# Optimization experiments

Hardware: AMD Instinct MI355X
Metric: run time of the kernel (lower is better)

## Reference

```python
import jax, jax.numpy as jnp
import numpy as np

ALPHA = 0.2  # leaky relu slope
NEG_BIG = -9000000000000000.0


def setup_inputs() -> dict:
    key = jax.random.key(0)
    k1, k2, k3, k4 = jax.random.split(key, 4)
    B, N, Fin, Fout = 8, 2048, 256, 256
    h = jax.random.normal(k1, (B, N, Fin), dtype=jnp.float32)
    adj = jax.random.randint(k2, (B, N, N), 0, 2, dtype=jnp.int32)
    # xavier_uniform with gain=1.414
    gain = 1.414
    limW = gain * np.sqrt(6.0 / (Fin + Fout))
    W = jax.random.uniform(k3, (Fin, Fout), dtype=jnp.float32, minval=-limW, maxval=limW)
    lima = gain * np.sqrt(6.0 / (2 * Fout + 1))
    a = jax.random.uniform(k4, (2 * Fout, 1), dtype=jnp.float32, minval=-lima, maxval=lima)
    return {"h": h, "adj": adj, "W": W, "a": a}


def reference(h, adj, W, a):
    # Wh: [B, N, F]
    Wh = jnp.matmul(h, W)
    Fout = W.shape[1]
    a1 = a[:Fout, 0]   # scores for source node i (repeat_interleave side)
    a2 = a[Fout:, 0]   # scores for target node j (repeat side)
    # e[b,i,j] = leakyrelu(Wh[b,i]@a1 + Wh[b,j]@a2)  -- decomposed, no O(N^2 * 2F) tensor
    s1 = jnp.einsum('bnf,f->bn', Wh, a1)  # [B, N]
    s2 = jnp.einsum('bnf,f->bn', Wh, a2)  # [B, N]
    e = jax.nn.leaky_relu(s1[:, :, None] + s2[:, None, :], negative_slope=ALPHA)
    masked = jnp.where(adj > 0, e, jnp.full_like(e, NEG_BIG))
    attention = jax.nn.softmax(masked, axis=2)  # dropout=0 (eval mode)
    h_prime = jnp.matmul(attention, Wh)  # [B, N, F]
    return jax.nn.elu(h_prime)
```

## Files before the change

kernel.cpp:

```cpp
#include <hip/hip_runtime.h>

typedef __attribute__((ext_vector_type(8))) short bhalf8;
typedef __attribute__((ext_vector_type(4))) float floatx4;

#define ALPHA_LR 0.2f

__device__ __forceinline__ unsigned short f2bf(float f) {
  union { float f; unsigned int u; } v; v.f = f;
  unsigned int r = v.u + 0x7fffu + ((v.u >> 16) & 1u);
  return (unsigned short)(r >> 16);
}
__device__ __forceinline__ float bf2f(unsigned short u) {
  union { unsigned int u; float f; } v; v.u = ((unsigned int)u) << 16;
  return v.f;
}
__device__ __forceinline__ void gld16(const void* g, void* l) {
  __builtin_amdgcn_global_load_lds((const __attribute__((address_space(1))) unsigned int*)g,
                                   (__attribute__((address_space(3))) unsigned int*)l,
                                   16, 0, 0);
}

__global__ void k0w_split(const float* __restrict__ W,
                          unsigned short* __restrict__ WThi,
                          unsigned short* __restrict__ WTlo,
                          unsigned int* __restrict__ s2maxEnc) {
  __shared__ float s[16][17];
  const int tx = threadIdx.x, ty = threadIdx.y;
  if (blockIdx.x == 0 && blockIdx.y == 0 && ty == 0 && tx < 8) s2maxEnc[tx] = 0u;
  const int n0 = blockIdx.x * 16, k0 = blockIdx.y * 16;
  s[ty][tx] = W[(k0 + ty) * 256 + n0 + tx];
  __syncthreads();
  float v = s[tx][ty];
  const int k = k0 + tx, n = n0 + ty;
  unsigned short hi = f2bf(v);
  unsigned short lo = f2bf(v - bf2f(hi));
  const int idx = (k >> 5) * 8192 + n * 32 + (k & 31);
  WThi[idx] = hi;
  WTlo[idx] = lo;
}

__global__ __launch_bounds__(512, 2) void k1_mfma(const float* __restrict__ h,
                                                  const unsigned short* __restrict__ Bhi_g,
                                                  const unsigned short* __restrict__ Blo_g,
                                                  const float* __restrict__ a_g,
                                                  unsigned short* __restrict__ WhPack,
                                                  float* __restrict__ s1,
                                                  float* __restrict__ s2,
                                                  unsigned int* __restrict__ s2maxEnc) {
  __shared__ unsigned short Ah[64 * 264], Al[64 * 264];
  __shared__ unsigned short Bh[2][8192], Bl[2][8192];
  __shared__ float s1red[64], s2red[64];
  const int t = threadIdx.x;
  const long r0 = (long)blockIdx.x * 64;
  const int wave = t >> 6, lane = t & 63;

  if (t < 64) { s1red[t] = 0.f; s2red[t] = 0.f; }

#pragma unroll
  for (int rep = 0; rep < 2; rep++) {
    const int off = wave * 1024 + rep * 512;
    gld16(Bhi_g + off + lane * 8, &Bh[0][off]);
    gld16(Blo_g + off + lane * 8, &Bl[0][off]);
  }

#pragma unroll
  for (int q = 0; q < 8; q++) {
    int idx = q * 512 + t;
    int row = idx >> 6, c4 = idx & 63;
    float4 x = *(const float4*)(h + (r0 + row) * 256 + c4 * 4);
    float xs[4] = {x.x, x.y, x.z, x.w};
    unsigned short hs[4], ls[4];
#pragma unroll
    for (int qq = 0; qq < 4; qq++) {
      hs[qq] = f2bf(xs[qq]);
      ls[qq] = f2bf(xs[qq] - bf2f(hs[qq]));
    }
    *(ushort4*)&Ah[row * 264 + c4 * 4] = (ushort4){hs[0], hs[1], hs[2], hs[3]};
    *(ushort4*)&Al[row * 264 + c4 * 4] = (ushort4){ls[0], ls[1], ls[2], ls[3]};
  }
  __syncthreads();

  const int wm = wave >> 2, wn = wave & 3;
  const int lhi = lane >> 4, llo = lane & 15;

  floatx4 acc[2][4];
#pragma unroll
  for (int mt = 0; mt < 2; mt++)
#pragma unroll
    for (int nt = 0; nt < 4; nt++) acc[mt][nt] = (floatx4){0.f, 0.f, 0.f, 0.f};

  for (int ks = 0; ks < 8; ks++) {
    const int cur = ks & 1, nxt = cur ^ 1, ksn = (ks + 1) & 7;
#pragma unroll
    for (int rep = 0; rep < 2; rep++) {
      const int off = wave * 1024 + rep * 512;
      gld16(Bhi_g + ksn * 8192 + off + lane * 8, &Bh[nxt][off]);
      gld16(Blo_g + ksn * 8192 + off + lane * 8, &Bl[nxt][off]);
    }

    const int k0 = ks * 32;
    bhalf8 ah[2], al[2], bh[4], bl[4];
#pragma unroll
    for (int mt = 0; mt < 2; mt++) {
      int ro = (wm * 32 + mt * 16 + llo) * 264 + k0 + lhi * 8;
      ah[mt] = *(const bhalf8*)&Ah[ro];
      al[mt] = *(const bhalf8*)&Al[ro];
    }
#pragma unroll
    for (int nt = 0; nt < 4; nt++) {
      int ro = (wn * 64 + nt * 16 + llo) * 32 + lhi * 8;
      bh[nt] = *(const bhalf8*)&Bh[cur][ro];
      bl[nt] = *(const bhalf8*)&Bl[cur][ro];
    }
#pragma unroll
    for (int mt = 0; mt < 2; mt++)
#pragma unroll
      for (int nt = 0; nt < 4; nt++) {
        acc[mt][nt] = __builtin_amdgcn_mfma_f32_16x16x32_bf16(ah[mt], bh[nt], acc[mt][nt], 0, 0, 0);
        acc[mt][nt] = __builtin_amdgcn_mfma_f32_16x16x32_bf16(ah[mt], bl[nt], acc[mt][nt], 0, 0, 0);
        acc[mt][nt] = __builtin_amdgcn_mfma_f32_16x16x32_bf16(al[mt], bh[nt], acc[mt][nt], 0, 0, 0);
      }
    __syncthreads();
  }

  float a1v[4], a2v[4];
#pragma unroll
  for (int nt = 0; nt < 4; nt++) {
    int f = wn * 64 + nt * 16 + llo;
    a1v[nt] = a_g[f];
    a2v[nt] = a_g[256 + f];
  }

  const int b = (int)(r0 >> 11);
  const int jt_base = (int)((r0 & 2047) >> 5);

#pragma unroll
  for (int mt = 0; mt < 2; mt++) {
    float p1[4], p2[4];
#pragma unroll
    for (int reg = 0; reg < 4; reg++) {
      p1[reg] = acc[mt][0][reg] * a1v[0] + acc[mt][1][reg] * a1v[1] +
                acc[mt][2][reg] * a1v[2] + acc[mt][3][reg] * a1v[3];
      p2[reg] = acc[mt][0][reg] * a2v[0] + acc[mt][1][reg] * a2v[1] +
                acc[mt][2][reg] * a2v[2] + acc[mt][3][reg] * a2v[3];
    }
#pragma unroll
    for (int off = 1; off < 16; off <<= 1) {
#pragma unroll
      for (int reg = 0; reg < 4; reg++) {
        p1[reg] += __shfl_xor(p1[reg], off);
        p2[reg] += __shfl_xor(p2[reg], off);
      }
    }
    if (llo == 0) {
#pragma unroll
      for (int reg = 0; reg < 4; reg++) {
        int il = wm * 32 + mt * 16 + lhi * 4 + reg;
        atomicAdd(&s1red[il], p1[reg]);
        atomicAdd(&s2red[il], p2[reg]);
      }
    }
#pragma unroll
    for (int nt = 0; nt < 4; nt++) {
      int f = wn * 64 + nt * 16 + llo;
      int jt = jt_base + wm;
      ushort4 pk = (ushort4){f2bf(acc[mt][nt][0]), f2bf(acc[mt][nt][1]),
                             f2bf(acc[mt][nt][2]), f2bf(acc[mt][nt][3])};
      *(ushort4*)&WhPack[((long)((b * 64 + jt) * 256 + f)) * 32 + mt * 16 + lhi * 4] = pk;
    }
  }

  __syncthreads();
  if (t < 64) {
    s1[r0 + t] = s1red[t];
    s2[r0 + t] = s2red[t];
    float v = s2red[t];
#pragma unroll
    for (int o = 32; o; o >>= 1) v = fmaxf(v, __shfl_xor(v, o));
    if (t == 0) {
      unsigned int u = __float_as_uint(v);
      unsigned int key = (u & 0x80000000u) ? ~u : (u | 0x80000000u);
      atomicMax(s2maxEnc + b, key);
    }
  }
}

__global__ __launch_bounds__(512, 2) void k3_attn(const unsigned short* __restrict__ WhPack,
                                                  const int* __restrict__ adj,
                                                  const float* __restrict__ s1g,
                                                  const float* __restrict__ s2g,
                                                  const unsigned int* __restrict__ s2maxEnc,
                                                  float* __restrict__ out) {
  const int t = threadIdx.x;
  const int lin = blockIdx.x;
  const int b = lin & 7;
  const int ig = lin >> 3;
  const long gr0 = (long)b * 2048 + ig * 64;

  const int wave = t >> 6, lane = t & 63;
  const int rg = wave >> 2, fg = wave & 3;
  const int llo = lane & 15, lhi = lane >> 4;

  __shared__ unsigned short WhL[2][16384];
  __shared__ unsigned short Pl[2][64 * 72];
  __shared__ float s2l[2048];
  __shared__ float lvv[64];

  const int pr = t >> 3;
  const int pq = t & 7;

  const float s1i = s1g[gr0 + pr];
  const unsigned int ek = s2maxEnc[b];
  const float s2max = (ek & 0x80000000u) ? __uint_as_float(ek & 0x7fffffffu)
                                         : __uint_as_float(~ek);
  const float xm = s1i + s2max;
  const float Mi = fmaxf(xm, ALPHA_LR * xm);
  const int* arow = adj + (gr0 + pr) * 2048 + pq * 8;

  const int gsrc8 = (((lane & 3) ^ ((lane >> 3) & 3))) * 8;
  const unsigned short* wsrcB =
      WhPack + (long)b * 524288 + wave * 512 + (lane >> 2) * 32 + gsrc8;

  const int boff = fg * 2048 + llo * 32 + (lhi ^ ((llo >> 1) & 3)) * 8;
  const int aoff = (rg * 32 + llo) * 72 + lhi * 8;

  *(float4*)&s2l[t * 4] = *(const float4*)(s2g + (long)b * 2048 + t * 4);
#pragma unroll
  for (int i = 0; i < 4; i++)
    gld16(wsrcB + i * 4096, &WhL[0][i * 4096 + wave * 512]);
  int4 a0A = *(const int4*)(arow);
  int4 a0B = *(const int4*)(arow + 4);
  int4 ajCA = *(const int4*)(arow + 64);
  int4 ajCB = *(const int4*)(arow + 68);
  __syncthreads();

  float lsum = 0.f;
  {
    int am[8] = {a0A.x, a0A.y, a0A.z, a0A.w, a0B.x, a0B.y, a0B.z, a0B.w};
    float4 sA = *(const float4*)&s2l[pq * 8];
    float4 sB = *(const float4*)&s2l[pq * 8 + 4];
    float xs[8] = {sA.x, sA.y, sA.z, sA.w, sB.x, sB.y, sB.z, sB.w};
    unsigned int pk[4];
    float e[8];
#pragma unroll
    for (int q = 0; q < 8; q++) {
      float x = s1i + xs[q];
      float lk = fmaxf(x, ALPHA_LR * x);
      float ee = __expf(lk - Mi);
      ee = (am[q] > 0) ? ee : 0.f;
      lsum += ee;
      e[q] = ee;
    }
#pragma unroll
    for (int q = 0; q < 4; q++)
      asm("v_cvt_pk_bf16_f32 %0, %1, %2" : "=v"(pk[q]) : "v"(e[2 * q]), "v"(e[2 * q + 1]));
    *(uint4*)&Pl[0][pr * 72 + pq * 8] = (uint4){pk[0], pk[1], pk[2], pk[3]};
  }
  __syncthreads();

  floatx4 acc[2][4];
#pragma unroll
  for (int mt = 0; mt < 2; mt++)
#pragma unroll
    for (int nt = 0; nt < 4; nt++) acc[mt][nt] = (floatx4){0.f, 0.f, 0.f, 0.f};

#pragma unroll 2
  for (int step = 0; step < 32; step++) {
    const int cur = step & 1, nxt = cur ^ 1;

    if (step < 31) {
      const long jb = (long)(step + 1) * 16384;
#pragma unroll
      for (int i = 0; i < 4; i++)
        gld16(wsrcB + jb + i * 4096, &WhL[nxt][i * 4096 + wave * 512]);
    }
    const int tp = (step < 30 ? step + 2 : 31) * 64;
    int4 ajNA = *(const int4*)(arow + tp);
    int4 ajNB = *(const int4*)(arow + tp + 4);
    __builtin_amdgcn_sched_barrier(0);

    if (step < 31) {
      int am[8] = {ajCA.x, ajCA.y, ajCA.z, ajCA.w, ajCB.x, ajCB.y, ajCB.z, ajCB.w};
      const int sbase = (step + 1) * 64 + pq * 8;
      float4 sA = *(const float4*)&s2l[sbase];
      float4 sB = *(const float4*)&s2l[sbase + 4];
      float xs[8] = {sA.x, sA.y, sA.z, sA.w, sB.x, sB.y, sB.z, sB.w};
      unsigned int pk[4];
      float e[8];
#pragma unroll
      for (int q = 0; q < 8; q++) {
        float x = s1i + xs[q];
        float lk = fmaxf(x, ALPHA_LR * x);
        float ee = __expf(lk - Mi);
        ee = (am[q] > 0) ? ee : 0.f;
        lsum += ee;
        e[q] = ee;
      }
#pragma unroll
      for (int q = 0; q < 4; q++)
        asm("v_cvt_pk_bf16_f32 %0, %1, %2" : "=v"(pk[q]) : "v"(e[2 * q]), "v"(e[2 * q + 1]));
      *(uint4*)&Pl[nxt][pr * 72 + pq * 8] = (uint4){pk[0], pk[1], pk[2], pk[3]};
    }
    ajCA = ajNA; ajCB = ajNB;

#pragma unroll
    for (int kk = 0; kk < 2; kk++) {
      bhalf8 aF[2], bF[4];
#pragma unroll
      for (int mt = 0; mt < 2; mt++)
        aF[mt] = *(const bhalf8*)&Pl[cur][aoff + mt * 1152 + kk * 32];
#pragma unroll
      for (int nt = 0; nt < 4; nt++)
        bF[nt] = *(const bhalf8*)&WhL[cur][kk * 8192 + nt * 512 + boff];
#pragma unroll
      for (int mt = 0; mt < 2; mt++)
#pragma unroll
        for (int nt = 0; nt < 4; nt++)
          acc[mt][nt] = __builtin_amdgcn_mfma_f32_16x16x32_bf16(aF[mt], bF[nt], acc[mt][nt], 0, 0, 0);
    }

    __syncthreads();
  }

  lsum += __shfl_xor(lsum, 1);
  lsum += __shfl_xor(lsum, 2);
  lsum += __shfl_xor(lsum, 4);
  if ((lane & 7) == 0) lvv[pr] = lsum;
  __syncthreads();

#pragma unroll
  for (int mt = 0; mt < 2; mt++) {
#pragma unroll
    for (int reg = 0; reg < 4; reg++) {
      const int rloc = rg * 32 + mt * 16 + lhi * 4 + reg;
      const float iv = 1.f / fmaxf(lvv[rloc], 1e-35f);
      const long orow = (gr0 + rloc) * 256 + fg * 64 + llo;
#pragma unroll
      for (int nt = 0; nt < 4; nt++) {
        float v = acc[mt][nt][reg] * iv;
        v = v > 0.f ? v : expm1f(v);
        out[orow + nt * 16] = v;
      }
    }
  }
}

extern "C" void kernel_launch(void* const* d_in, const int* in_sizes, int n_in,
                              void* d_out, int out_size, void* d_ws, size_t ws_size,
                              hipStream_t stream) {
  const float* h = (const float*)d_in[0];
  const int* adj = (const int*)d_in[1];
  const float* W = (const float*)d_in[2];
  const float* a = (const float*)d_in[3];
  float* out = (float*)d_out;

  char* ws = (char*)d_ws;
  unsigned short* WhPack = (unsigned short*)ws;
  unsigned short* WThi = (unsigned short*)(ws + 8388608);
  unsigned short* WTlo = (unsigned short*)(ws + 8519680);
  float* s1 = (float*)(ws + 8650752);
  float* s2 = (float*)(ws + 8716288);
  unsigned int* s2maxEnc = (unsigned int*)(ws + 8781824);

  hipLaunchKernelGGL(k0w_split, dim3(16, 16), dim3(16, 16), 0, stream, W, WThi, WTlo, s2maxEnc);
  hipLaunchKernelGGL(k1_mfma, dim3(256), dim3(512), 0, stream, h, WThi, WTlo, a,
                     WhPack, s1, s2, s2maxEnc);
  hipLaunchKernelGGL(k3_attn, dim3(256), dim3(512), 0, stream, WhPack, adj,
                     s1, s2, s2maxEnc, out);
}
```

Baseline: 243.1 us.

## Compute attention scores from h·(W·a) and drop low-part A MFMA

Precomputes W·a1 and W·a2 in the weight-prep kernel, so the scores s1 and s2 are computed in fp32 straight from h during the A-tile load, replacing the post-GEMM epilogue reduction with its shared-memory atomics. It also removes the low-order bf16 split of h, cutting the MFMA count per tile from three to two and halving the A-side shared memory. In exchange the Wh GEMM loses the h-residual correction term, which lowers the precision of Wh, and each wave does extra shuffle reductions during the load phase.

```diff
diff --git a/kernel.cpp b/kernel.cpp
--- a/kernel.cpp
+++ b/kernel.cpp
@@ -21,11 +21,36 @@
 }
 
 __global__ void k0w_split(const float* __restrict__ W,
+                          const float* __restrict__ a_g,
                           unsigned short* __restrict__ WThi,
                           unsigned short* __restrict__ WTlo,
-                          unsigned int* __restrict__ s2maxEnc) {
+                          unsigned int* __restrict__ s2maxEnc,
+                          float* __restrict__ Wa) {
+  const int tx = threadIdx.x, ty = threadIdx.y;
+  if (blockIdx.y == 16) {
+    __shared__ float r1[16][17], r2[16][17];
+    const int k = blockIdx.x * 16 + ty;
+    const float* wr = W + k * 256 + tx * 16;
+    float p1 = 0.f, p2 = 0.f;
+#pragma unroll
+    for (int j = 0; j < 16; j++) {
+      float w = wr[j];
+      p1 += w * a_g[tx * 16 + j];
+      p2 += w * a_g[256 + tx * 16 + j];
+    }
+    r1[ty][tx] = p1;
+    r2[ty][tx] = p2;
+    __syncthreads();
+    if (tx == 0) {
+      float v1 = 0.f, v2 = 0.f;
+#pragma unroll
+      for (int j = 0; j < 16; j++) { v1 += r1[ty][j]; v2 += r2[ty][j]; }
+      Wa[k] = v1;
+      Wa[256 + k] = v2;
+    }
+    return;
+  }
   __shared__ float s[16][17];
-  const int tx = threadIdx.x, ty = threadIdx.y;
   if (blockIdx.x == 0 && blockIdx.y == 0 && ty == 0 && tx < 8) s2maxEnc[tx] = 0u;
   const int n0 = blockIdx.x * 16, k0 = blockIdx.y * 16;
   s[ty][tx] = W[(k0 + ty) * 256 + n0 + tx];
@@ -42,19 +67,16 @@
 __global__ __launch_bounds__(512, 2) void k1_mfma(const float* __restrict__ h,
                                                   const unsigned short* __restrict__ Bhi_g,
                                                   const unsigned short* __restrict__ Blo_g,
-                                                  const float* __restrict__ a_g,
+                                                  const float* __restrict__ Wa,
                                                   unsigned short* __restrict__ WhPack,
                                                   float* __restrict__ s1,
                                                   float* __restrict__ s2,
                                                   unsigned int* __restrict__ s2maxEnc) {
-  __shared__ unsigned short Ah[64 * 264], Al[64 * 264];
+  __shared__ unsigned short Ah[64 * 264];
   __shared__ unsigned short Bh[2][8192], Bl[2][8192];
-  __shared__ float s1red[64], s2red[64];
   const int t = threadIdx.x;
   const long r0 = (long)blockIdx.x * 64;
   const int wave = t >> 6, lane = t & 63;
-
-  if (t < 64) { s1red[t] = 0.f; s2red[t] = 0.f; }
 
 #pragma unroll
   for (int rep = 0; rep < 2; rep++) {
@@ -63,20 +85,35 @@
     gld16(Blo_g + off + lane * 8, &Bl[0][off]);
   }
 
+  const int c4 = t & 63;
+  const float4 wa1 = *(const float4*)(Wa + c4 * 4);
+  const float4 wa2 = *(const float4*)(Wa + 256 + c4 * 4);
+  float s2mx = -3.4e38f;
+
 #pragma unroll
   for (int q = 0; q < 8; q++) {
-    int idx = q * 512 + t;
-    int row = idx >> 6, c4 = idx & 63;
+    const int row = q * 8 + wave;
     float4 x = *(const float4*)(h + (r0 + row) * 256 + c4 * 4);
-    float xs[4] = {x.x, x.y, x.z, x.w};
-    unsigned short hs[4], ls[4];
-#pragma unroll
-    for (int qq = 0; qq < 4; qq++) {
-      hs[qq] = f2bf(xs[qq]);
-      ls[qq] = f2bf(xs[qq] - bf2f(hs[qq]));
-    }
+    unsigned short hs[4] = {f2bf(x.x), f2bf(x.y), f2bf(x.z), f2bf(x.w)};
     *(ushort4*)&Ah[row * 264 + c4 * 4] = (ushort4){hs[0], hs[1], hs[2], hs[3]};
-    *(ushort4*)&Al[row * 264 + c4 * 4] = (ushort4){ls[0], ls[1], ls[2], ls[3]};
+    float p1 = x.x * wa1.x + x.y * wa1.y + x.z * wa1.z + x.w * wa1.w;
+    float p2 = x.x * wa2.x + x.y * wa2.y + x.z * wa2.z + x.w * wa2.w;
+#pragma unroll
+    for (int off = 1; off < 64; off <<= 1) {
+      p1 += __shfl_xor(p1, off);
+      p2 += __shfl_xor(p2, off);
+    }
+    if (lane == 0) {
+      s1[r0 + row] = p1;
+      s2[r0 + row] = p2;
+    }
+    s2mx = fmaxf(s2mx, p2);
+  }
+  const int b = (int)(r0 >> 11);
+  if (lane == 0) {
+    unsigned int u = __float_as_uint(s2mx);
+    unsigned int key = (u & 0x80000000u) ? ~u : (u | 0x80000000u);
+    atomicMax(s2maxEnc + b, key);
   }
   __syncthreads();
 
@@ -99,12 +136,11 @@
     }
 
     const int k0 = ks * 32;
-    bhalf8 ah[2], al[2], bh[4], bl[4];
+    bhalf8 ah[2], bh[4], bl[4];
 #pragma unroll
     for (int mt = 0; mt < 2; mt++) {
       int ro = (wm * 32 + mt * 16 + llo) * 264 + k0 + lhi * 8;
       ah[mt] = *(const bhalf8*)&Ah[ro];
-      al[mt] = *(const bhalf8*)&Al[ro];
     }
 #pragma unroll
     for (int nt = 0; nt < 4; nt++) {
@@ -118,48 +154,14 @@
       for (int nt = 0; nt < 4; nt++) {
         acc[mt][nt] = __builtin_amdgcn_mfma_f32_16x16x32_bf16(ah[mt], bh[nt], acc[mt][nt], 0, 0, 0);
         acc[mt][nt] = __builtin_amdgcn_mfma_f32_16x16x32_bf16(ah[mt], bl[nt], acc[mt][nt], 0, 0, 0);
-        acc[mt][nt] = __builtin_amdgcn_mfma_f32_16x16x32_bf16(al[mt], bh[nt], acc[mt][nt], 0, 0, 0);
       }
     __syncthreads();
   }
 
-  float a1v[4], a2v[4];
-#pragma unroll
-  for (int nt = 0; nt < 4; nt++) {
-    int f = wn * 64 + nt * 16 + llo;
-    a1v[nt] = a_g[f];
-    a2v[nt] = a_g[256 + f];
-  }
-
-  const int b = (int)(r0 >> 11);
   const int jt_base = (int)((r0 & 2047) >> 5);
 
 #pragma unroll
   for (int mt = 0; mt < 2; mt++) {
-    float p1[4], p2[4];
-#pragma unroll
-    for (int reg = 0; reg < 4; reg++) {
-      p1[reg] = acc[mt][0][reg] * a1v[0] + acc[mt][1][reg] * a1v[1] +
-                acc[mt][2][reg] * a1v[2] + acc[mt][3][reg] * a1v[3];
-      p2[reg] = acc[mt][0][reg] * a2v[0] + acc[mt][1][reg] * a2v[1] +
-                acc[mt][2][reg] * a2v[2] + acc[mt][3][reg] * a2v[3];
-    }
-#pragma unroll
-    for (int off = 1; off < 16; off <<= 1) {
-#pragma unroll
-      for (int reg = 0; reg < 4; reg++) {
-        p1[reg] += __shfl_xor(p1[reg], off);
-        p2[reg] += __shfl_xor(p2[reg], off);
-      }
-    }
-    if (llo == 0) {
-#pragma unroll
-      for (int reg = 0; reg < 4; reg++) {
-        int il = wm * 32 + mt * 16 + lhi * 4 + reg;
-        atomicAdd(&s1red[il], p1[reg]);
-        atomicAdd(&s2red[il], p2[reg]);
-      }
-    }
 #pragma unroll
     for (int nt = 0; nt < 4; nt++) {
       int f = wn * 64 + nt * 16 + llo;
@@ -167,20 +169,6 @@
       ushort4 pk = (ushort4){f2bf(acc[mt][nt][0]), f2bf(acc[mt][nt][1]),
                              f2bf(acc[mt][nt][2]), f2bf(acc[mt][nt][3])};
       *(ushort4*)&WhPack[((long)((b * 64 + jt) * 256 + f)) * 32 + mt * 16 + lhi * 4] = pk;
-    }
-  }
-
-  __syncthreads();
-  if (t < 64) {
-    s1[r0 + t] = s1red[t];
-    s2[r0 + t] = s2red[t];
-    float v = s2red[t];
-#pragma unroll
-    for (int o = 32; o; o >>= 1) v = fmaxf(v, __shfl_xor(v, o));
-    if (t == 0) {
-      unsigned int u = __float_as_uint(v);
-      unsigned int key = (u & 0x80000000u) ? ~u : (u | 0x80000000u);
-      atomicMax(s2maxEnc + b, key);
     }
   }
 }
@@ -361,9 +349,11 @@
   float* s1 = (float*)(ws + 8650752);
   float* s2 = (float*)(ws + 8716288);
   unsigned int* s2maxEnc = (unsigned int*)(ws + 8781824);
-
-  hipLaunchKernelGGL(k0w_split, dim3(16, 16), dim3(16, 16), 0, stream, W, WThi, WTlo, s2maxEnc);
-  hipLaunchKernelGGL(k1_mfma, dim3(256), dim3(512), 0, stream, h, WThi, WTlo, a,
+  float* Wa = (float*)(ws + 8781888);
+
+  hipLaunchKernelGGL(k0w_split, dim3(16, 17), dim3(16, 16), 0, stream, W, a,
+                     WThi, WTlo, s2maxEnc, Wa);
+  hipLaunchKernelGGL(k1_mfma, dim3(256), dim3(512), 0, stream, h, WThi, WTlo, Wa,
                      WhPack, s1, s2, s2maxEnc);
   hipLaunchKernelGGL(k3_attn, dim3(256), dim3(512), 0, stream, WhPack, adj,
                      s1, s2, s2maxEnc, out);
```

Result: slower. 262.7 us (+8.1%).
